# Kernel optimization log

Measured on AMD Instinct MI355X. Metric: run time of the kernel, lower is better.

The kernel has to match this reference:

```python
import jax, jax.numpy as jnp
import numpy as np

N_NODES = 50000
N_EDGES = 800000
IN_DIM = 128
OUT_DIM = 128
NEG_INIT = -1e9  # matches torch fill_(-1e9) init for scatter amax
LEAKY_SLOPE = 0.01  # nn.LeakyReLU default


def setup_inputs() -> dict:
    key = jax.random.key(0)
    ks = jax.random.split(key, 8)
    x = jax.random.normal(ks[0], (N_NODES, IN_DIM), dtype=jnp.float32)
    edge_index = jax.random.randint(ks[1], (2, N_EDGES), 0, N_NODES, dtype=jnp.int64)
    edge_weight = jax.random.uniform(ks[2], (N_EDGES,), dtype=jnp.float32)
    # MLP params (nn.Linear default init: U(-1/sqrt(fan_in), 1/sqrt(fan_in)))
    s1 = 1.0 / np.sqrt(IN_DIM)
    s2 = 1.0 / np.sqrt(OUT_DIM)
    w1 = jax.random.uniform(ks[3], (OUT_DIM, IN_DIM), minval=-s1, maxval=s1, dtype=jnp.float32)
    b1 = jax.random.uniform(ks[4], (OUT_DIM,), minval=-s1, maxval=s1, dtype=jnp.float32)
    w2 = jax.random.uniform(ks[5], (OUT_DIM, OUT_DIM), minval=-s2, maxval=s2, dtype=jnp.float32)
    b2 = jax.random.uniform(ks[6], (OUT_DIM,), minval=-s2, maxval=s2, dtype=jnp.float32)
    eps = jnp.zeros((1,), dtype=jnp.float32)
    return {"x": x, "edge_index": edge_index, "edge_weight": edge_weight,
            "w1": w1, "b1": b1, "w2": w2, "b2": b2, "eps": eps}


def reference(x, edge_index, edge_weight, w1, b1, w2, b2, eps):
    src = edge_index[0]
    dst = edge_index[1]
    # gather + optional edge-weight scale: [E, D]
    messages = x[src] * edge_weight[:, None]
    # scatter-max to dst; init at -1e9 so include_self=False semantics hold
    agg = jnp.full(x.shape, NEG_INIT, dtype=x.dtype).at[dst].max(messages)
    agg = jnp.where(agg == NEG_INIT, jnp.zeros_like(agg), agg)  # isolated nodes -> 0
    h = (1.0 + eps) * x + agg  # eps broadcasts ([1])
    h = h @ w1.T + b1
    h = jnp.where(h >= 0, h, LEAKY_SLOPE * h)  # LeakyReLU
    out = h @ w2.T + b2
    return out
```

## Files before the change

### kernel.cpp

```cpp
#include <hip/hip_runtime.h>
#include <stdint.h>

#define NN 50000
#define NE 800000
#define D  128
#define NEG_INIT -1e9f
#define CAP 64
#define OVF_CAP 131072

#define CNT_OFF     64
#define OVF_CNT_OFF 50064
#define OVF_OFF     50068
#define BKT_OFF     312320
#define XBF_OFF     3512320
#define WBF_OFF     6712320

#define HSTRIDE 136

#define FILL_BLKS 3125
#define PX_BLKS   6250
#define PW_BLKS   32

typedef __attribute__((ext_vector_type(8))) short short8;
typedef __attribute__((ext_vector_type(4))) float float4v;

__device__ __forceinline__ float b2f(uint16_t u) {
    union { uint32_t u; float f; } v; v.u = ((uint32_t)u) << 16; return v.f;
}
__device__ __forceinline__ uint16_t f2b(float f) {
    union { float f; uint32_t u; } v; v.f = f;
    uint32_t r = v.u + 0x7fffu + ((v.u >> 16) & 1u);
    return (uint16_t)(r >> 16);
}

__device__ __forceinline__ void block_probe(const uint16_t* __restrict__ xraw,
                                            const int* __restrict__ eraw,
                                            int* sflags) {
    int t = threadIdx.x;
    if (t < 64) {
        float v0 = b2f(xraw[2 * t]);
        float v1 = b2f(xraw[2 * t + 1]);
        int bad = (!(v0 > -1e4f && v0 < 1e4f)) || (!(v1 > -1e4f && v1 < 1e4f));
        unsigned long long bm = __ballot(bad);
        int nz = (t < 32) ? (eraw[2 * t + 1] != 0) : 0;
        unsigned long long im = __ballot(nz);
        if (t == 0) { sflags[0] = bm ? 1 : 0; sflags[1] = im ? 0 : 1; }
    }
    __syncthreads();
}

__global__ __launch_bounds__(256) void prep_fill_kernel(
    const uint16_t* __restrict__ xraw,
    const int*      __restrict__ eraw,
    const uint16_t* __restrict__ ewraw,
    const uint16_t* __restrict__ w1raw,
    const uint16_t* __restrict__ w2raw,
    int* __restrict__ ws)
{
    __shared__ int sflags[2];
    block_probe(xraw, eraw, sflags);
    const int f32 = sflags[0], i64 = sflags[1];

    int bid = blockIdx.x;
    if (bid < FILL_BLKS) {
        int e = bid * 256 + threadIdx.x;
        int src, dst;
        if (i64) {
            const long long* e64 = (const long long*)eraw;
            src = (int)e64[e];
            dst = (int)e64[NE + e];
        } else {
            src = eraw[e];
            dst = eraw[NE + e];
        }
        if ((unsigned)src >= NN || (unsigned)dst >= NN) return;
        uint w = f32 ? (uint)f2b(((const float*)ewraw)[e]) : (uint)ewraw[e];
        uint entry = (w << 16) | (uint)src;
        int slot = atomicAdd(ws + CNT_OFF + dst, 1);
        if (slot < CAP) {
            ((uint*)(ws + BKT_OFF))[(size_t)dst * CAP + slot] = entry;
        } else {
            int o = atomicAdd(ws + OVF_CNT_OFF, 1);
            if (o < OVF_CAP) {
                ws[OVF_OFF + 2 * o]     = dst;
                ws[OVF_OFF + 2 * o + 1] = (int)entry;
            }
        }
    } else if (bid < FILL_BLKS + PX_BLKS) {
        int i4 = ((bid - FILL_BLKS) * 256 + threadIdx.x) * 4;
        ushort* dst = (ushort*)(ws + XBF_OFF);
        if (f32) {
            float4 v = *(const float4*)((const float*)xraw + i4);
            ushort4 o; o.x = f2b(v.x); o.y = f2b(v.y); o.z = f2b(v.z); o.w = f2b(v.w);
            *(ushort4*)(dst + i4) = o;
        } else {
            *(ushort4*)(dst + i4) = *(const ushort4*)(xraw + i4);
        }
    } else {
        int i4 = ((bid - FILL_BLKS - PX_BLKS) * 256 + threadIdx.x) * 4;
        const uint16_t* src = (i4 < 16384) ? w1raw : w2raw;
        int off = i4 & 16383;
        ushort* dst = (ushort*)(ws + WBF_OFF);
        if (f32) {
            float4 v = *(const float4*)((const float*)src + off);
            ushort4 o; o.x = f2b(v.x); o.y = f2b(v.y); o.z = f2b(v.z); o.w = f2b(v.w);
            *(ushort4*)(dst + i4) = o;
        } else {
            *(ushort4*)(dst + i4) = *(const ushort4*)(src + off);
        }
    }
}

__global__ __launch_bounds__(256) void gmlp_kernel(
    const uint16_t* __restrict__ xraw,
    const int*      __restrict__ eraw,
    const uint16_t* __restrict__ b1raw,
    const uint16_t* __restrict__ b2raw,
    const uint16_t* __restrict__ epsraw,
    const int* __restrict__ ws,
    uint16_t* __restrict__ outraw)
{
    __shared__ int    sflags[2];
    __shared__ uint   tl[16 * (HSTRIDE / 2)];
    __shared__ ushort hl[16 * HSTRIDE];

    block_probe(xraw, eraw, sflags);
    const int f32 = sflags[0];

    const int tid  = threadIdx.x;
    const int wave = tid >> 6;
    const int lane = tid & 63;
    const int m    = lane & 15;
    const int quad = lane >> 4;
    const int node0 = blockIdx.x * 16;

    const ushort* w1b = (const ushort*)(ws + WBF_OFF);
    const ushort* w2b = w1b + 16384;
    const uint*   xbf = (const uint*)(ws + XBF_OFF);
    const uint*   bkt = (const uint*)(ws + BKT_OFF);

    const float eps1 = 1.0f + (f32 ? ((const float*)epsraw)[0] : b2f(epsraw[0]));

    for (int j = 0; j < 4; ++j) {
        int nl = wave * 4 + j;
        int n  = node0 + nl;
        int cnt_raw = ws[CNT_OFF + n];
        int cnt = (cnt_raw < CAP) ? cnt_raw : CAP;

        float m0[16], m1[16];
        #pragma unroll
        for (int u = 0; u < 16; ++u) { m0[u] = NEG_INIT; m1[u] = NEG_INIT; }

        const uint* brow = bkt + (size_t)n * CAP;
        for (int i = 0; i < cnt; i += 16) {
            uint4 q[4];
            #pragma unroll
            for (int qq = 0; qq < 4; ++qq) q[qq] = *(const uint4*)(brow + i + qq * 4);
            #pragma unroll
            for (int u = 0; u < 16; ++u) {
                uint e0 = ((const uint*)q)[u];
                bool ok = (i + u) < cnt;
                uint idx = ok ? (e0 & 0xffffu) : 0u;
                uint v = xbf[idx * 64 + lane];
                float w  = b2f((uint16_t)(e0 >> 16));
                float p0 = b2f((uint16_t)v) * w;
                float p1 = b2f((uint16_t)(v >> 16)) * w;
                m0[u] = fmaxf(m0[u], ok ? p0 : NEG_INIT);
                m1[u] = fmaxf(m1[u], ok ? p1 : NEG_INIT);
            }
        }
        if (cnt_raw > CAP) {
            int novf = ws[OVF_CNT_OFF];
            if (novf > OVF_CAP) novf = OVF_CAP;
            for (int o = 0; o < novf; ++o) {
                if (ws[OVF_OFF + 2 * o] == n) {
                    uint e0 = (uint)ws[OVF_OFF + 2 * o + 1];
                    uint v  = xbf[(e0 & 0xffff) * 64 + lane];
                    float w = b2f((uint16_t)(e0 >> 16));
                    m0[0] = fmaxf(m0[0], b2f((uint16_t)v) * w);
                    m1[0] = fmaxf(m1[0], b2f((uint16_t)(v >> 16)) * w);
                }
            }
        }
        #pragma unroll
        for (int u = 8; u > 0; u >>= 1)
            #pragma unroll
            for (int v2 = 0; v2 < u; ++v2) {
                m0[v2] = fmaxf(m0[v2], m0[v2 + u]);
                m1[v2] = fmaxf(m1[v2], m1[v2 + u]);
            }
        float mx = m0[0], my = m1[0];
        if (cnt_raw == 0) { mx = 0.f; my = 0.f; }

        uint xv = xbf[(size_t)n * 64 + lane];
        float t0 = eps1 * b2f((uint16_t)xv) + mx;
        float t1 = eps1 * b2f((uint16_t)(xv >> 16)) + my;
        tl[nl * (HSTRIDE / 2) + lane] = (uint)f2b(t0) | ((uint)f2b(t1) << 16);
    }
    __syncthreads();

    short8 a[4];
    {
        const ushort* arow = (const ushort*)tl + m * HSTRIDE + quad * 8;
        #pragma unroll
        for (int kb = 0; kb < 4; ++kb) a[kb] = *(const short8*)(arow + kb * 32);
    }

    #pragma unroll
    for (int t = 0; t < 2; ++t) {
        int ct = wave * 2 + t;
        float4v c = {0.f, 0.f, 0.f, 0.f};
        const ushort* brow = w1b + (size_t)(ct * 16 + m) * 128 + quad * 8;
        #pragma unroll
        for (int kb = 0; kb < 4; ++kb)
            c = __builtin_amdgcn_mfma_f32_16x16x32_bf16(a[kb], *(const short8*)(brow + kb * 32), c, 0, 0, 0);
        float bias = f32 ? ((const float*)b1raw)[ct * 16 + m] : b2f(b1raw[ct * 16 + m]);
        #pragma unroll
        for (int r = 0; r < 4; ++r) {
            float v = c[r] + bias;
            v = (v >= 0.f) ? v : 0.01f * v;
            hl[(quad * 4 + r) * HSTRIDE + ct * 16 + m] = f2b(v);
        }
    }
    __syncthreads();

    short8 ah[4];
    {
        const ushort* hrow = hl + m * HSTRIDE + quad * 8;
        #pragma unroll
        for (int kb = 0; kb < 4; ++kb) ah[kb] = *(const short8*)(hrow + kb * 32);
    }

    #pragma unroll
    for (int t = 0; t < 2; ++t) {
        int ct = wave * 2 + t;
        float4v c = {0.f, 0.f, 0.f, 0.f};
        const ushort* brow = w2b + (size_t)(ct * 16 + m) * 128 + quad * 8;
        #pragma unroll
        for (int kb = 0; kb < 4; ++kb)
            c = __builtin_amdgcn_mfma_f32_16x16x32_bf16(ah[kb], *(const short8*)(brow + kb * 32), c, 0, 0, 0);
        float bias = f32 ? ((const float*)b2raw)[ct * 16 + m] : b2f(b2raw[ct * 16 + m]);
        #pragma unroll
        for (int r = 0; r < 4; ++r) {
            float v = c[r] + bias;
            size_t o = (size_t)(node0 + quad * 4 + r) * 128 + ct * 16 + m;
            if (f32) ((float*)outraw)[o] = v;
            else     outraw[o] = f2b(v);
        }
    }
}

extern "C" void kernel_launch(void* const* d_in, const int* in_sizes, int n_in,
                              void* d_out, int out_size, void* d_ws, size_t ws_size,
                              hipStream_t stream) {
    const uint16_t* x    = (const uint16_t*)d_in[0];
    const int*      eidx = (const int*)     d_in[1];
    const uint16_t* ew   = (const uint16_t*)d_in[2];
    const uint16_t* w1   = (const uint16_t*)d_in[3];
    const uint16_t* b1   = (const uint16_t*)d_in[4];
    const uint16_t* w2   = (const uint16_t*)d_in[5];
    const uint16_t* b2   = (const uint16_t*)d_in[6];
    const uint16_t* eps  = (const uint16_t*)d_in[7];
    uint16_t*       out  = (uint16_t*)d_out;
    int* ws = (int*)d_ws;

    hipMemsetAsync((char*)d_ws + (size_t)CNT_OFF * 4, 0,
                   (size_t)(NN + 1) * 4, stream);
    prep_fill_kernel<<<FILL_BLKS + PX_BLKS + PW_BLKS, 256, 0, stream>>>(
        x, eidx, ew, w1, w2, ws);
    gmlp_kernel<<<NN / 16, 256, 0, stream>>>(x, eidx, b1, b2, eps, ws, out);
}
```

Measured before the change: 210.9 us.

## Pad degree counters, sentinel-fill buckets, and drop per-edge predicates in gather

Each per-node degree counter now sits on its own 64-byte stride, so concurrent atomics from the fill stage should land on separate cache lines. The bucket array is pre-filled with 0xFF, which makes unused slots decode as a NaN weight. fmaxf ignores NaN, so the gather loop can drop its validity predicate, clamping the source index instead. Counts are also loaded up front for all four nodes of a wave. The cost is an extra 12.8 MB memset per call and a padded counter region that is larger to zero and touches more cache lines.

```diff
diff --git a/kernel.cpp b/kernel.cpp
--- a/kernel.cpp
+++ b/kernel.cpp
@@ -9,11 +9,12 @@
 #define OVF_CAP 131072
 
 #define CNT_OFF     64
-#define OVF_CNT_OFF 50064
-#define OVF_OFF     50068
-#define BKT_OFF     312320
-#define XBF_OFF     3512320
-#define WBF_OFF     6712320
+#define CNT_STRIDE  16
+#define OVF_CNT_OFF (CNT_OFF + NN * CNT_STRIDE)
+#define OVF_OFF     (OVF_CNT_OFF + 4)
+#define BKT_OFF     1062400
+#define XBF_OFF     (BKT_OFF + NN * CAP)
+#define WBF_OFF     (XBF_OFF + NN * (D / 2))
 
 #define HSTRIDE 136
 
@@ -26,6 +27,9 @@
 
 __device__ __forceinline__ float b2f(uint16_t u) {
     union { uint32_t u; float f; } v; v.u = ((uint32_t)u) << 16; return v.f;
+}
+__device__ __forceinline__ float ubits(uint32_t u) {
+    union { uint32_t u; float f; } v; v.u = u; return v.f;
 }
 __device__ __forceinline__ uint16_t f2b(float f) {
     union { float f; uint32_t u; } v; v.f = f;
@@ -76,7 +80,7 @@
         if ((unsigned)src >= NN || (unsigned)dst >= NN) return;
         uint w = f32 ? (uint)f2b(((const float*)ewraw)[e]) : (uint)ewraw[e];
         uint entry = (w << 16) | (uint)src;
-        int slot = atomicAdd(ws + CNT_OFF + dst, 1);
+        int slot = atomicAdd(ws + CNT_OFF + dst * CNT_STRIDE, 1);
         if (slot < CAP) {
             ((uint*)(ws + BKT_OFF))[(size_t)dst * CAP + slot] = entry;
         } else {
@@ -141,10 +145,15 @@
 
     const float eps1 = 1.0f + (f32 ? ((const float*)epsraw)[0] : b2f(epsraw[0]));
 
+    int cr[4];
+    #pragma unroll
+    for (int j = 0; j < 4; ++j)
+        cr[j] = ws[CNT_OFF + (wave * 4 + j + node0) * CNT_STRIDE];
+
     for (int j = 0; j < 4; ++j) {
         int nl = wave * 4 + j;
         int n  = node0 + nl;
-        int cnt_raw = ws[CNT_OFF + n];
+        int cnt_raw = cr[j];
         int cnt = (cnt_raw < CAP) ? cnt_raw : CAP;
 
         float m0[16], m1[16];
@@ -158,15 +167,15 @@
             for (int qq = 0; qq < 4; ++qq) q[qq] = *(const uint4*)(brow + i + qq * 4);
             #pragma unroll
             for (int u = 0; u < 16; ++u) {
-                uint e0 = ((const uint*)q)[u];
-                bool ok = (i + u) < cnt;
-                uint idx = ok ? (e0 & 0xffffu) : 0u;
+                uint e0  = ((const uint*)q)[u];
+                uint idx = e0 & 0xffffu;
+                idx = min(idx, (uint)(NN - 1));
                 uint v = xbf[idx * 64 + lane];
-                float w  = b2f((uint16_t)(e0 >> 16));
-                float p0 = b2f((uint16_t)v) * w;
-                float p1 = b2f((uint16_t)(v >> 16)) * w;
-                m0[u] = fmaxf(m0[u], ok ? p0 : NEG_INIT);
-                m1[u] = fmaxf(m1[u], ok ? p1 : NEG_INIT);
+                float w  = ubits(e0 & 0xffff0000u);
+                float p0 = ubits(v << 16) * w;
+                float p1 = ubits(v & 0xffff0000u) * w;
+                m0[u] = fmaxf(m0[u], p0);
+                m1[u] = fmaxf(m1[u], p1);
             }
         }
         if (cnt_raw > CAP) {
@@ -265,7 +274,9 @@
     int* ws = (int*)d_ws;
 
     hipMemsetAsync((char*)d_ws + (size_t)CNT_OFF * 4, 0,
-                   (size_t)(NN + 1) * 4, stream);
+                   ((size_t)NN * CNT_STRIDE + 1) * 4, stream);
+    hipMemsetAsync((char*)d_ws + (size_t)BKT_OFF * 4, 0xFF,
+                   (size_t)NN * CAP * 4, stream);
     prep_fill_kernel<<<FILL_BLKS + PX_BLKS + PW_BLKS, 256, 0, stream>>>(
         x, eidx, ew, w1, w2, ws);
     gmlp_kernel<<<NN / 16, 256, 0, stream>>>(x, eidx, b1, b2, eps, ws, out);
```

After: 203.4 us. 3.6% less time.
